# Optimization experiments

Hardware: AMD Instinct MI355X
Metric: run time of the kernel (lower is better)

Reference implementation:

```python
import jax, jax.numpy as jnp
import numpy as np

N_HEADS = 16
D_MODEL = 1024
D_K = D_MODEL // N_HEADS
B, T = 2, 2048


def setup_inputs() -> dict:
    key = jax.random.key(0)
    ks = jax.random.split(key, 12)
    s = 1.0 / np.sqrt(D_MODEL)
    inp = {
        "q": jax.random.normal(ks[0], (B, T, D_MODEL), jnp.float32),
        "k": jax.random.normal(ks[1], (B, T, D_MODEL), jnp.float32),
        "v": jax.random.normal(ks[2], (B, T, D_MODEL), jnp.float32),
        # weights stored as [in, out] (torch Linear weight transposed)
        "Wq": jax.random.normal(ks[3], (D_MODEL, D_MODEL), jnp.float32) * s,
        "bq": jax.random.normal(ks[4], (D_MODEL,), jnp.float32) * s,
        "Wk": jax.random.normal(ks[5], (D_MODEL, D_MODEL), jnp.float32) * s,
        "bk": jax.random.normal(ks[6], (D_MODEL,), jnp.float32) * s,
        "Wv": jax.random.normal(ks[7], (D_MODEL, D_MODEL), jnp.float32) * s,
        "bv": jax.random.normal(ks[8], (D_MODEL,), jnp.float32) * s,
        "Wo": jax.random.normal(ks[9], (D_MODEL, D_MODEL), jnp.float32) * s,
        "bo": jax.random.normal(ks[10], (D_MODEL,), jnp.float32) * s,
        "alpha": jnp.ones((1, N_HEADS, 1, 1), jnp.float32) * 10.0,
    }
    return inp


def reference(q, k, v, Wq, bq, Wk, bk, Wv, bv, Wo, bo, alpha):
    Bsz, Tlen, _ = q.shape

    def proj(x, W, b):
        # [B,T,D] -> [B,H,T,d_k]
        y = x @ W + b
        return y.reshape(Bsz, Tlen, N_HEADS, D_K).transpose(0, 2, 1, 3)

    qh = proj(q, Wq, bq)
    kh = proj(k, Wk, bk)
    vh = proj(v, Wv, bv)

    scores = jnp.einsum("bhqd,bhkd->bhqk", qh, kh)  # [B,H,T,T]
    norm_q = jnp.linalg.norm(qh, axis=-1)  # [B,H,T]
    norm_k = jnp.linalg.norm(kh, axis=-1)  # [B,H,T]
    D_udps = (norm_q[..., :, None] + norm_k[..., None, :]) ** 2  # [B,H,T,T]
    D_safe = jnp.where(D_udps == 0.0, jnp.inf, D_udps)
    scores = alpha * 4.0 * scores / D_safe
    attn = jax.nn.softmax(scores, axis=-1)
    out = jnp.einsum("bhqk,bhkd->bhqd", attn, vh)
    out = out.transpose(0, 2, 1, 3).reshape(Bsz, Tlen, D_MODEL)
    return out @ Wo + bo
```

## Files before the change

### kernel.cpp

```cpp
#include <hip/hip_runtime.h>
#include <hip/hip_bf16.h>

#define N_HEADS 16
#define D_MODEL 1024
#define D_K     64
#define B_SZ    2
#define T_LEN   2048
#define M_ROWS  (B_SZ * T_LEN)

typedef __bf16 bf16;
typedef __bf16 bf16x4 __attribute__((ext_vector_type(4)));
typedef __bf16 bf16x8 __attribute__((ext_vector_type(8)));
typedef float  f32x4  __attribute__((ext_vector_type(4)));
typedef unsigned int u32;

__device__ __forceinline__ void gload16(const bf16* g, bf16* l) {
    __builtin_amdgcn_global_load_lds(
        (const __attribute__((address_space(1))) u32*)g,
        (__attribute__((address_space(3))) u32*)l, 16, 0, 0);
}

#define WAIT_VM(N) asm volatile("s_waitcnt vmcnt(" #N ")" ::: "memory")

__global__ void wt_kernel(const float* __restrict__ W0, const float* __restrict__ W1,
                          const float* __restrict__ W2, const float* __restrict__ W3,
                          bf16* __restrict__ T0, bf16* __restrict__ T1,
                          bf16* __restrict__ T2, bf16* __restrict__ T3) {
    __shared__ float tile[32][33];
    const int z = blockIdx.z;
    const float* W = (z == 0) ? W0 : (z == 1) ? W1 : (z == 2) ? W2 : W3;
    bf16* Wt       = (z == 0) ? T0 : (z == 1) ? T1 : (z == 2) ? T2 : T3;
    const int tx = threadIdx.x, ty = threadIdx.y;
    const int x0 = blockIdx.x * 32, y0 = blockIdx.y * 32;
    for (int yy = ty; yy < 32; yy += 8)
        tile[yy][tx] = W[(size_t)(y0 + yy) * D_MODEL + x0 + tx];
    __syncthreads();
    for (int yy = ty; yy < 32; yy += 8)
        Wt[(size_t)(x0 + yy) * D_MODEL + y0 + tx] = (bf16)tile[tx][yy];
}

__global__ void conv3_kernel(const float* __restrict__ q, const float* __restrict__ k,
                             const float* __restrict__ v,
                             bf16* __restrict__ qb, bf16* __restrict__ kb,
                             bf16* __restrict__ vb) {
    const int z = blockIdx.y;
    const float* X = (z == 0) ? q : (z == 1) ? k : v;
    bf16* Y        = (z == 0) ? qb : (z == 1) ? kb : vb;
    const size_t i = ((size_t)blockIdx.x * 256 + threadIdx.x) * 8;
    const float4 v0 = *(const float4*)&X[i];
    const float4 v1 = *(const float4*)&X[i + 4];
    bf16x8 y;
    y[0]=(bf16)v0.x; y[1]=(bf16)v0.y; y[2]=(bf16)v0.z; y[3]=(bf16)v0.w;
    y[4]=(bf16)v1.x; y[5]=(bf16)v1.y; y[6]=(bf16)v1.z; y[7]=(bf16)v1.w;
    *(bf16x8*)&Y[i] = y;
}

__global__ __launch_bounds__(256, 3) void proj_kernel(
    const bf16* __restrict__ qb, const bf16* __restrict__ kb, const bf16* __restrict__ vb,
    const bf16* __restrict__ WtQ, const bf16* __restrict__ WtK, const bf16* __restrict__ WtV,
    const float* __restrict__ bqp, const float* __restrict__ bkp, const float* __restrict__ bvp,
    bf16* __restrict__ qh, bf16* __restrict__ kh, bf16* __restrict__ vt,
    float* __restrict__ nq, float* __restrict__ nk)
{
    __shared__ bf16 As[3][128 * 32];
    __shared__ bf16 Bs[3][128 * 32];

    const int hw      = blockIdx.x;
    const int logical = (hw & 7) * 96 + (hw >> 3);
    const int z       = logical >> 8;
    const int r       = logical & 255;
    const int m0      = (r >> 3) * 128;
    const int n0      = (r & 7) * 128;

    const bf16*  A    = (z == 0) ? qb  : (z == 1) ? kb  : vb;
    const bf16*  Bt   = (z == 0) ? WtQ : (z == 1) ? WtK : WtV;
    const float* bias = (z == 0) ? bqp : (z == 1) ? bkp : bvp;
    bf16* Out         = (z == 0) ? qh  : (z == 1) ? kh  : vt;

    const int tid = threadIdx.x, lane = tid & 63, w = tid >> 6;
    const int wm = w >> 1, wn = w & 1, g = lane >> 4, c = lane & 15;

    const int srow = w * 32 + (lane >> 2);
    const int scol = (lane & 3) * 8;
    const bf16* Ag = A  + (size_t)(m0 + srow) * D_MODEL + scol;
    const bf16* Bg = Bt + (size_t)(n0 + srow) * D_MODEL + scol;

    f32x4 acc[4][4] = {};

#define PSTAGE(buf, kk)                                                         \
    do {                                                                        \
        gload16(Ag + (kk),                  &As[buf][(w * 32) * 32]);           \
        gload16(Ag + 16 * D_MODEL + (kk),   &As[buf][(w * 32 + 16) * 32]);      \
        gload16(Bg + (kk),                  &Bs[buf][(w * 32) * 32]);           \
        gload16(Bg + 16 * D_MODEL + (kk),   &Bs[buf][(w * 32 + 16) * 32]);      \
    } while (0)

    PSTAGE(0, 0);
    PSTAGE(1, 32);
    WAIT_VM(4);
    __builtin_amdgcn_s_barrier();

    int cur = 0;
    for (int t = 0; t < 32; ++t) {
        if (t + 2 < 32) {
            int pre = cur + 2; if (pre >= 3) pre -= 3;
            PSTAGE(pre, (t + 2) * 32);
        }

        bf16x8 a[4], b[4];
        #pragma unroll
        for (int i = 0; i < 4; i++) a[i] = *(const bf16x8*)&As[cur][(wm*64 + i*16 + c) * 32 + g*8];
        #pragma unroll
        for (int j = 0; j < 4; j++) b[j] = *(const bf16x8*)&Bs[cur][(wn*64 + j*16 + c) * 32 + g*8];

        __builtin_amdgcn_s_setprio(1);
        if (z != 2) {
            #pragma unroll
            for (int i = 0; i < 4; i++)
                #pragma unroll
                for (int j = 0; j < 4; j++)
                    acc[i][j] = __builtin_amdgcn_mfma_f32_16x16x32_bf16(a[i], b[j], acc[i][j], 0, 0, 0);
        } else {
            #pragma unroll
            for (int i = 0; i < 4; i++)
                #pragma unroll
                for (int j = 0; j < 4; j++)
                    acc[i][j] = __builtin_amdgcn_mfma_f32_16x16x32_bf16(b[j], a[i], acc[i][j], 0, 0, 0);
        }
        __builtin_amdgcn_s_setprio(0);

        if (t + 2 < 32) { WAIT_VM(4); }
        else            { WAIT_VM(0); }
        __builtin_amdgcn_s_barrier();
        cur = (cur + 1 == 3) ? 0 : cur + 1;
    }
#undef PSTAGE

    if (z != 2) {
        float* nrm = (z == 0) ? nq : nk;
        const int h_ = (n0 >> 6) + wn;
        #pragma unroll
        for (int i = 0; i < 4; i++)
            #pragma unroll
            for (int r4 = 0; r4 < 4; r4++) {
                const int mrow = m0 + wm*64 + i*16 + g*4 + r4;
                const int b_ = mrow >> 11, t_ = mrow & (T_LEN - 1);
                float ss = 0.f;
                #pragma unroll
                for (int j = 0; j < 4; j++) {
                    const int ncol = n0 + wn*64 + j*16 + c;
                    const float y = acc[i][j][r4] + bias[ncol];
                    Out[(((size_t)(b_*N_HEADS + h_))*T_LEN + t_)*D_K + j*16 + c] = (bf16)y;
                    ss += y * y;
                }
                ss += __shfl_xor(ss, 1, 64);
                ss += __shfl_xor(ss, 2, 64);
                ss += __shfl_xor(ss, 4, 64);
                ss += __shfl_xor(ss, 8, 64);
                if (c == 0)
                    nrm[((size_t)(b_*N_HEADS + h_))*T_LEN + t_] = sqrtf(ss);
            }
    } else {
        #pragma unroll
        for (int i = 0; i < 4; i++)
            #pragma unroll
            for (int j = 0; j < 4; j++)
                #pragma unroll
                for (int r4 = 0; r4 < 4; r4++) {
                    const int nrow = n0 + wn*64 + j*16 + g*4 + r4;
                    const int mcol = m0 + wm*64 + i*16 + c;
                    const float y = acc[i][j][r4] + bias[nrow];
                    const int b_ = mcol >> 11, t_ = mcol & (T_LEN - 1);
                    const int h2 = nrow >> 6,  d_ = nrow & (D_K - 1);
                    Out[(((size_t)(b_*N_HEADS + h2))*D_K + d_)*T_LEN + t_] = (bf16)y;
                }
    }
}

#define KVB 64

__global__ __launch_bounds__(512, 4) void attn_kernel(
    const bf16* __restrict__ qh, const bf16* __restrict__ kh, const bf16* __restrict__ vt,
    const float* __restrict__ nq, const float* __restrict__ nk,
    const float* __restrict__ alpha, bf16* __restrict__ ao)
{
    __shared__ bf16 Ks[3][KVB * D_K];
    __shared__ bf16 Vs[3][KVB * D_K];
    __shared__ bf16 plds[8][16][72];

    const int bid     = blockIdx.x;
    const int logical = (bid & 7) * 64 + (bid >> 3);
    const int bh      = logical >> 4;
    const int q0b     = (logical & 15) * 128;

    const int tid  = threadIdx.x;
    const int w    = tid >> 6;
    const int lane = tid & 63;
    const int g    = lane >> 4, c = lane & 15;
    const int myq  = q0b + w * 16 + c;
    const int sw   = (c & 7) << 4;

    const int srow = tid >> 3;
    const int sgb  = (((tid & 7) ^ (srow & 7)) << 4);

    const bf16* Q  = qh + (size_t)bh * T_LEN * D_K;
    const bf16* K  = kh + (size_t)bh * T_LEN * D_K;
    const bf16* V  = vt + (size_t)bh * D_K * T_LEN;
    const float* NK = nk + (size_t)bh * T_LEN;

    const float al   = alpha[bh & (N_HEADS - 1)];
    const float a4   = al * 4.0f * 1.44269504f;
    const float negM = -(al * 1.44269504f) - 1e-4f;

    const bf16x8 bq0 = *(const bf16x8*)&Q[(size_t)myq * D_K + g*8];
    const bf16x8 bq1 = *(const bf16x8*)&Q[(size_t)myq * D_K + 32 + g*8];
    const float nq_own = nq[(size_t)bh * T_LEN + myq];

    bf16x8 ones;
    #pragma unroll
    for (int e = 0; e < 8; e++) ones[e] = (bf16)1.0f;

    f32x4 o[4] = {};
    f32x4 o4  = {};

#define AKSTAGE(buf, kn)                                                                          \
    do {                                                                                          \
        gload16((const bf16*)((const char*)&K[(size_t)((kn) + srow) * D_K] + sgb), &Ks[buf][w * 512]); \
        gload16((const bf16*)((const char*)&V[(size_t)srow * T_LEN + (kn)] + sgb), &Vs[buf][w * 512]); \
    } while (0)

#define SM(cb)                                                                  \
    do {                                                                        \
        bf16x4 pk;                                                              \
        pk[0] = (bf16)__builtin_amdgcn_exp2f(                                   \
            __builtin_fmaf(S[cb][0], rd2[cb][0], negM));                        \
        pk[1] = (bf16)__builtin_amdgcn_exp2f(                                   \
            __builtin_fmaf(S[cb][1], rd2[cb][1], negM));                        \
        pk[2] = (bf16)__builtin_amdgcn_exp2f(                                   \
            __builtin_fmaf(S[cb][2], rd2[cb][2], negM));                        \
        pk[3] = (bf16)__builtin_amdgcn_exp2f(                                   \
            __builtin_fmaf(S[cb][3], rd2[cb][3], negM));                        \
        *(bf16x4*)&plds[w][c][(cb)*16 + g*4] = pk;                              \
    } while (0)

#define PV(ks)                                                                  \
    do {                                                                        \
        const bf16x8 pb = *(const bf16x8*)&plds[w][c][(ks)*32 + g*8];           \
        __builtin_amdgcn_s_setprio(1);                                          \
        _Pragma("unroll")                                                       \
        for (int f = 0; f < 4; f++)                                             \
            o[f] = __builtin_amdgcn_mfma_f32_16x16x32_bf16(vbr[ks][f], pb, o[f], 0, 0, 0); \
        o4 = __builtin_amdgcn_mfma_f32_16x16x32_bf16(ones, pb, o4, 0, 0, 0);    \
        __builtin_amdgcn_s_setprio(0);                                          \
    } while (0)

    AKSTAGE(0, 0);
    AKSTAGE(1, KVB);
    WAIT_VM(2);
    __builtin_amdgcn_s_barrier();

    const int NT = T_LEN / KVB;
    int cur = 0;
    for (int t = 0; t < NT; ++t) {
        const int k0 = t * KVB;

        float4 nk4[4];
        #pragma unroll
        for (int cb = 0; cb < 4; cb++) nk4[cb] = *(const float4*)&NK[k0 + cb*16 + g*4];
        __builtin_amdgcn_sched_barrier(0);

        if (t + 2 < NT) {
            int pre = cur + 2; if (pre >= 3) pre -= 3;
            AKSTAGE(pre, k0 + 2*KVB);
        }

        f32x4 S[4];
        __builtin_amdgcn_s_setprio(1);
        #pragma unroll
        for (int cb = 0; cb < 4; cb++) {
            const char* kbase = (const char*)&Ks[cur][(size_t)(cb*16 + c) * D_K];
            const bf16x8 ka = *(const bf16x8*)(kbase + ((g*16) ^ sw));
            const bf16x8 kb = *(const bf16x8*)(kbase + ((64 + g*16) ^ sw));
            f32x4 s = {};
            s = __builtin_amdgcn_mfma_f32_16x16x32_bf16(ka, bq0, s, 0, 0, 0);
            s = __builtin_amdgcn_mfma_f32_16x16x32_bf16(kb, bq1, s, 0, 0, 0);
            S[cb] = s;
        }
        __builtin_amdgcn_s_setprio(0);

        bf16x8 vbr[2][4];
        #pragma unroll
        for (int ks = 0; ks < 2; ks++)
            #pragma unroll
            for (int f = 0; f < 4; f++) {
                const char* vbase = (const char*)&Vs[cur][(size_t)(f*16 + c) * D_K];
                vbr[ks][f] = *(const bf16x8*)(vbase + ((ks*64 + g*16) ^ sw));
            }

        float rd2[4][4];
        #pragma unroll
        for (int cb = 0; cb < 4; cb++) {
            const float nkr[4] = {nk4[cb].x, nk4[cb].y, nk4[cb].z, nk4[cb].w};
            #pragma unroll
            for (int r = 0; r < 4; r++) {
                const float den = nq_own + nkr[r];
                const float rr  = __builtin_amdgcn_rcpf(den);
                rd2[cb][r] = (a4 * rr) * rr;
            }
        }

        SM(0); SM(1);
        PV(0);
        SM(2); SM(3);
        PV(1);

        if (t + 2 < NT) { WAIT_VM(2); }
        else            { WAIT_VM(0); }
        __builtin_amdgcn_s_barrier();
        cur = (cur + 1 == 3) ? 0 : cur + 1;
    }
#undef AKSTAGE
#undef SM
#undef PV

    const int b_ = bh >> 4, h_ = bh & 15;
    const float inv = 1.0f / o4[0];
    #pragma unroll
    for (int f = 0; f < 4; f++) {
        bf16x4 w4;
        #pragma unroll
        for (int r = 0; r < 4; r++) w4[r] = (bf16)(o[f][r] * inv);
        *(bf16x4*)&ao[((size_t)(b_*T_LEN + myq))*D_MODEL + h_*D_K + f*16 + g*4] = w4;
    }
}

__global__ __launch_bounds__(256, 4) void gemmo_kernel(
    const bf16* __restrict__ A, const bf16* __restrict__ Bt,
    const float* __restrict__ bias, float* __restrict__ Out)
{
    __shared__ bf16 As[3][64 * 32];
    __shared__ bf16 Bs[3][128 * 32];

    const int hw      = blockIdx.x;
    const int logical = (hw & 7) * 64 + (hw >> 3);
    const int m0      = (logical >> 3) * 64;
    const int n0      = (logical & 7) * 128;

    const int tid = threadIdx.x, lane = tid & 63, w = tid >> 6;
    const int wm = w >> 1, wn = w & 1, g = lane >> 4, c = lane & 15;

    const int arow = w * 16 + (lane >> 2);
    const int brow = w * 32 + (lane >> 2);
    const int scol = (lane & 3) * 8;
    const bf16* Ag = A  + (size_t)(m0 + arow) * D_MODEL + scol;
    const bf16* Bg = Bt + (size_t)(n0 + brow) * D_MODEL + scol;

    f32x4 acc[2][4] = {};

#define OSTAGE(buf, kk)                                                         \
    do {                                                                        \
        gload16(Ag + (kk),                &As[buf][(w * 16) * 32]);             \
        gload16(Bg + (kk),                &Bs[buf][(w * 32) * 32]);             \
        gload16(Bg + 16 * D_MODEL + (kk), &Bs[buf][(w * 32 + 16) * 32]);        \
    } while (0)

    OSTAGE(0, 0);
    OSTAGE(1, 32);
    WAIT_VM(3);
    __builtin_amdgcn_s_barrier();

    int cur = 0;
    for (int t = 0; t < 32; ++t) {
        if (t + 2 < 32) {
            int pre = cur + 2; if (pre >= 3) pre -= 3;
            OSTAGE(pre, (t + 2) * 32);
        }

        bf16x8 a[2], b[4];
        #pragma unroll
        for (int i = 0; i < 2; i++) a[i] = *(const bf16x8*)&As[cur][(wm*32 + i*16 + c) * 32 + g*8];
        #pragma unroll
        for (int j = 0; j < 4; j++) b[j] = *(const bf16x8*)&Bs[cur][(wn*64 + j*16 + c) * 32 + g*8];

        __builtin_amdgcn_s_setprio(1);
        #pragma unroll
        for (int i = 0; i < 2; i++)
            #pragma unroll
            for (int j = 0; j < 4; j++)
                acc[i][j] = __builtin_amdgcn_mfma_f32_16x16x32_bf16(a[i], b[j], acc[i][j], 0, 0, 0);
        __builtin_amdgcn_s_setprio(0);

        if (t + 2 < 32) { WAIT_VM(3); }
        else            { WAIT_VM(0); }
        __builtin_amdgcn_s_barrier();
        cur = (cur + 1 == 3) ? 0 : cur + 1;
    }
#undef OSTAGE

    #pragma unroll
    for (int i = 0; i < 2; i++)
        #pragma unroll
        for (int j = 0; j < 4; j++) {
            const int ncol = n0 + wn*64 + j*16 + c;
            const float bb = bias[ncol];
            #pragma unroll
            for (int r = 0; r < 4; r++) {
                const int mrow = m0 + wm*32 + i*16 + g*4 + r;
                Out[(size_t)mrow * D_MODEL + ncol] = acc[i][j][r] + bb;
            }
        }
}

extern "C" void kernel_launch(void* const* d_in, const int* in_sizes, int n_in,
                              void* d_out, int out_size, void* d_ws, size_t ws_size,
                              hipStream_t stream) {
    const float* q     = (const float*)d_in[0];
    const float* k     = (const float*)d_in[1];
    const float* v     = (const float*)d_in[2];
    const float* Wq    = (const float*)d_in[3];
    const float* bq    = (const float*)d_in[4];
    const float* Wk    = (const float*)d_in[5];
    const float* bk    = (const float*)d_in[6];
    const float* Wv    = (const float*)d_in[7];
    const float* bv    = (const float*)d_in[8];
    const float* Wo    = (const float*)d_in[9];
    const float* bo    = (const float*)d_in[10];
    const float* alpha = (const float*)d_in[11];

    char* ws = (char*)d_ws;
    const size_t WBYTES = (size_t)D_MODEL * D_MODEL * sizeof(bf16);
    const size_t HBYTES = (size_t)B_SZ * N_HEADS * T_LEN * D_K * sizeof(bf16);
    const size_t NBYTES = (size_t)B_SZ * N_HEADS * T_LEN * sizeof(float);
    bf16* WtQ = (bf16*)ws;  ws += WBYTES;
    bf16* WtK = (bf16*)ws;  ws += WBYTES;
    bf16* WtV = (bf16*)ws;  ws += WBYTES;
    bf16* WtO = (bf16*)ws;  ws += WBYTES;
    bf16* qh  = (bf16*)ws;  ws += HBYTES;
    bf16* kh  = (bf16*)ws;  ws += HBYTES;
    bf16* vt  = (bf16*)ws;  ws += HBYTES;
    float* nq = (float*)ws; ws += NBYTES;
    float* nk = (float*)ws; ws += NBYTES;
    bf16* ao  = (bf16*)ws;  ws += HBYTES;
    bf16* qb  = (bf16*)ws;  ws += HBYTES;
    bf16* kb  = (bf16*)ws;  ws += HBYTES;
    bf16* vb  = ao;

    wt_kernel<<<dim3(32, 32, 4), dim3(32, 8), 0, stream>>>(
        Wq, Wk, Wv, Wo, WtQ, WtK, WtV, WtO);

    conv3_kernel<<<dim3(M_ROWS * D_MODEL / 8 / 256, 3), 256, 0, stream>>>(
        q, k, v, qb, kb, vb);

    proj_kernel<<<768, 256, 0, stream>>>(
        qb, kb, vb, WtQ, WtK, WtV, bq, bk, bv, qh, kh, vt, nq, nk);

    attn_kernel<<<512, 512, 0, stream>>>(qh, kh, vt, nq, nk, alpha, ao);

    gemmo_kernel<<<512, 256, 0, stream>>>(ao, WtO, bo, (float*)d_out);
}
```

Measured before the change: 149.7 us.

## Load K tiles directly into registers and double-buffer V in LDS

The attention kernel stops staging K through shared memory. Each wave now loads its K fragments and the key norms straight from global memory into registers, one tile ahead. V keeps the async global-to-LDS path but goes from a triple buffer to a double buffer, with the wait count adjusted for the new mix of outstanding loads. This removes the K LDS traffic and cuts LDS footprint, which may raise occupancy. In exchange, every wave re-fetches the same K tile from cache, the prefetch distance drops from two tiles to one, and register pressure rises.

```diff
diff --git a/kernel.cpp b/kernel.cpp
--- a/kernel.cpp
+++ b/kernel.cpp
@@ -184,8 +184,7 @@
     const float* __restrict__ nq, const float* __restrict__ nk,
     const float* __restrict__ alpha, bf16* __restrict__ ao)
 {
-    __shared__ bf16 Ks[3][KVB * D_K];
-    __shared__ bf16 Vs[3][KVB * D_K];
+    __shared__ bf16 Vs[2][KVB * D_K];
     __shared__ bf16 plds[8][16][72];
 
     const int bid     = blockIdx.x;
@@ -223,10 +222,24 @@
     f32x4 o[4] = {};
     f32x4 o4  = {};
 
-#define AKSTAGE(buf, kn)                                                                          \
-    do {                                                                                          \
-        gload16((const bf16*)((const char*)&K[(size_t)((kn) + srow) * D_K] + sgb), &Ks[buf][w * 512]); \
-        gload16((const bf16*)((const char*)&V[(size_t)srow * T_LEN + (kn)] + sgb), &Vs[buf][w * 512]); \
+#define VSTAGE(buf, kn)                                                                           \
+    gload16((const bf16*)((const char*)&V[(size_t)srow * T_LEN + (kn)] + sgb), &Vs[buf][w * 512])
+
+#define KLOAD(kn)                                                               \
+    do {                                                                        \
+        _Pragma("unroll")                                                       \
+        for (int cb = 0; cb < 4; cb++) {                                        \
+            const bf16* Kr = &K[(size_t)((kn) + cb*16 + c) * D_K];              \
+            kr0[cb] = *(const bf16x8*)&Kr[g*8];                                 \
+            kr1[cb] = *(const bf16x8*)&Kr[32 + g*8];                            \
+        }                                                                       \
+    } while (0)
+
+#define NKLOAD(kn)                                                              \
+    do {                                                                        \
+        _Pragma("unroll")                                                       \
+        for (int cb = 0; cb < 4; cb++)                                          \
+            nk4[cb] = *(const float4*)&NK[(kn) + cb*16 + g*4];                  \
     } while (0)
 
 #define SM(cb)                                                                  \
@@ -254,48 +267,30 @@
         __builtin_amdgcn_s_setprio(0);                                          \
     } while (0)
 
-    AKSTAGE(0, 0);
-    AKSTAGE(1, KVB);
-    WAIT_VM(2);
+    bf16x8 kr0[4], kr1[4];
+    float4 nk4[4];
+
+    VSTAGE(0, 0);
+    KLOAD(0);
+    NKLOAD(0);
+    WAIT_VM(0);
     __builtin_amdgcn_s_barrier();
 
     const int NT = T_LEN / KVB;
     int cur = 0;
     for (int t = 0; t < NT; ++t) {
-        const int k0 = t * KVB;
-
-        float4 nk4[4];
-        #pragma unroll
-        for (int cb = 0; cb < 4; cb++) nk4[cb] = *(const float4*)&NK[k0 + cb*16 + g*4];
-        __builtin_amdgcn_sched_barrier(0);
-
-        if (t + 2 < NT) {
-            int pre = cur + 2; if (pre >= 3) pre -= 3;
-            AKSTAGE(pre, k0 + 2*KVB);
-        }
+        const int kn = (t + 1) * KVB;
 
         f32x4 S[4];
         __builtin_amdgcn_s_setprio(1);
         #pragma unroll
         for (int cb = 0; cb < 4; cb++) {
-            const char* kbase = (const char*)&Ks[cur][(size_t)(cb*16 + c) * D_K];
-            const bf16x8 ka = *(const bf16x8*)(kbase + ((g*16) ^ sw));
-            const bf16x8 kb = *(const bf16x8*)(kbase + ((64 + g*16) ^ sw));
             f32x4 s = {};
-            s = __builtin_amdgcn_mfma_f32_16x16x32_bf16(ka, bq0, s, 0, 0, 0);
-            s = __builtin_amdgcn_mfma_f32_16x16x32_bf16(kb, bq1, s, 0, 0, 0);
+            s = __builtin_amdgcn_mfma_f32_16x16x32_bf16(kr0[cb], bq0, s, 0, 0, 0);
+            s = __builtin_amdgcn_mfma_f32_16x16x32_bf16(kr1[cb], bq1, s, 0, 0, 0);
             S[cb] = s;
         }
         __builtin_amdgcn_s_setprio(0);
-
-        bf16x8 vbr[2][4];
-        #pragma unroll
-        for (int ks = 0; ks < 2; ks++)
-            #pragma unroll
-            for (int f = 0; f < 4; f++) {
-                const char* vbase = (const char*)&Vs[cur][(size_t)(f*16 + c) * D_K];
-                vbr[ks][f] = *(const bf16x8*)(vbase + ((ks*64 + g*16) ^ sw));
-            }
 
         float rd2[4][4];
         #pragma unroll
@@ -309,17 +304,32 @@
             }
         }
 
+        if (t + 1 < NT) VSTAGE(cur ^ 1, kn);
+        __builtin_amdgcn_sched_barrier(0);
+        if (t + 1 < NT) { KLOAD(kn); NKLOAD(kn); }
+
+        bf16x8 vbr[2][4];
+        #pragma unroll
+        for (int ks = 0; ks < 2; ks++)
+            #pragma unroll
+            for (int f = 0; f < 4; f++) {
+                const char* vbase = (const char*)&Vs[cur][(size_t)(f*16 + c) * D_K];
+                vbr[ks][f] = *(const bf16x8*)(vbase + ((ks*64 + g*16) ^ sw));
+            }
+
         SM(0); SM(1);
         PV(0);
         SM(2); SM(3);
         PV(1);
 
-        if (t + 2 < NT) { WAIT_VM(2); }
+        if (t + 1 < NT) { WAIT_VM(12); }
         else            { WAIT_VM(0); }
         __builtin_amdgcn_s_barrier();
-        cur = (cur + 1 == 3) ? 0 : cur + 1;
+        cur ^= 1;
     }
-#undef AKSTAGE
+#undef VSTAGE
+#undef KLOAD
+#undef NKLOAD
 #undef SM
 #undef PV
 
```

Measured after the change: 362.5 us. +142.1%, slower.
